# Performance work log

Measured on AMD Instinct MI355X. Metric: run time of the kernel, lower is better.

Reference implementation:

```python
import jax, jax.numpy as jnp
import numpy as np
from jax import lax

B, L, DIN, DOUT, K = 8, 4096, 256, 256, 3


def _gates(x, W, b, k):
    # x: [B, L, Din] -> conv over time, channels-first like torch Conv1d
    xt = jnp.transpose(x, (0, 2, 1))  # [B, Din, L]
    pad = (k - 1) // 2
    g = lax.conv_general_dilated(xt, W, window_strides=(1,), padding=[(pad, pad)],
                                 dimension_numbers=("NCH", "OIH", "NCH"))
    g = g + b[None, :, None]
    g = jnp.transpose(g, (0, 2, 1))  # [B, L, 3*Dout]
    f, o, z = jnp.split(g, 3, axis=-1)
    return jax.nn.sigmoid(f), jax.nn.sigmoid(o), jnp.tanh(z)


def _fo_pool(f, z, init_cell, reverse):
    # c_t = f_t * c_{t-1} + (1 - f_t) * z_t ; scan over time axis
    fT = jnp.transpose(f, (1, 0, 2))  # [L, B, D]
    zT = jnp.transpose(z, (1, 0, 2))

    def step(c, fz):
        ft, zt = fz
        c = ft * c + (1.0 - ft) * zt
        return c, c

    _, cells = lax.scan(step, init_cell, (fT, zT), reverse=reverse)
    return jnp.transpose(cells, (1, 0, 2))  # [B, L, D]


def setup_inputs() -> dict:
    key = jax.random.key(0)
    k1, k2, k3, k4, k5, k6 = jax.random.split(key, 6)
    scale_in = 1.0 / np.sqrt(DIN * K)
    inp = {
        "input": jax.random.normal(k1, (B, L, DIN), dtype=jnp.float32),
        "lengths": jnp.full((B,), L, dtype=jnp.int64) if False else jax.random.randint(k2, (B,), 1, L + 1),
        "W_fwd": jax.random.uniform(k3, (3 * DOUT, DIN, K), dtype=jnp.float32, minval=-scale_in, maxval=scale_in),
        "b_fwd": jax.random.uniform(k4, (3 * DOUT,), dtype=jnp.float32, minval=-scale_in, maxval=scale_in),
        "W_bwd": jax.random.uniform(k5, (3 * DOUT, DIN, K), dtype=jnp.float32, minval=-scale_in, maxval=scale_in),
        "b_bwd": jax.random.uniform(k6, (3 * DOUT,), dtype=jnp.float32, minval=-scale_in, maxval=scale_in),
    }
    return inp


def reference(input, lengths, W_fwd, b_fwd, W_bwd, b_bwd):
    init_cell = jnp.zeros((input.shape[0], DOUT), dtype=input.dtype)

    # forward direction
    f, o, z = _gates(input, W_fwd, b_fwd, K)
    cell = _fo_pool(f, z, init_cell, reverse=False)
    hidden = cell * o

    # backward direction
    fr, orr, zr = _gates(input, W_bwd, b_bwd, K)
    rcell = _fo_pool(fr, zr, init_cell, reverse=True)
    rhidden = rcell * orr

    output = jnp.concatenate([hidden, rhidden], axis=-1)  # [B, L, 2*Dout]
    last_h = jnp.concatenate([hidden[:, -1, :], rhidden[:, -1, :]], axis=-1)
    last_c = jnp.concatenate([cell[:, -1, :], rcell[:, -1, :]], axis=-1)
    return output, last_h, last_c
```

## Files before the change

kernel.cpp:

```cpp
#include <hip/hip_runtime.h>
#include <hip/hip_bf16.h>
#include <hip/hip_fp16.h>

#define B_     8
#define L_     4096
#define DIN    256
#define DOUT   256
#define NGATE  1536
#define KDIM   768
#define LP     (L_ + 2)
#define CHUNK  32
#define NCHUNK (L_ / CHUNK)

typedef short    short8  __attribute__((ext_vector_type(8)));
typedef __bf16   bf16x8  __attribute__((ext_vector_type(8)));
typedef float    floatx4 __attribute__((ext_vector_type(4)));
typedef _Float16 half4   __attribute__((ext_vector_type(4)));

__device__ __forceinline__ float fast_sigmoid(float x) {
    return __builtin_amdgcn_rcpf(1.f + __expf(-x));
}
__device__ __forceinline__ float fast_tanh(float x) {
    return 1.f - 2.f * __builtin_amdgcn_rcpf(1.f + __expf(2.f * x));
}
__device__ __forceinline__ unsigned short f2bf(float x) {
    unsigned u = __float_as_uint(x);
    u += 0x7FFF + ((u >> 16) & 1);
    return (unsigned short)(u >> 16);
}
__device__ __forceinline__ void gload16(const unsigned short* g, unsigned short* l) {
    __builtin_amdgcn_global_load_lds((const __attribute__((address_space(1))) void*)g,
                                     (__attribute__((address_space(3))) void*)l,
                                     16, 0, 0);
}

__device__ __forceinline__ int gate_noff(int n) {
    return (n >> 7) * 32768 + ((n >> 6) & 1) * 4096 + ((n >> 4) & 3) * 1024 + (n & 15) * 4;
}
__device__ __forceinline__ int gate_toff(int b, int t) {
    return (b * 16 + (t >> 8)) * 393216 + ((t >> 6) & 3) * 8192
         + ((t >> 4) & 3) * 256 + ((t >> 2) & 3) * 64;
}

#define NXB ((B_ * LP * 64 + 255) / 256)
#define NWB ((NGATE * KDIM + 255) / 256)
__global__ void prep_all(const float* __restrict__ x, unsigned short* __restrict__ Xp,
                         const float* __restrict__ Wf, const float* __restrict__ bf_,
                         const float* __restrict__ Wb, const float* __restrict__ bb,
                         unsigned short* __restrict__ Wc, float* __restrict__ bc) {
    if (blockIdx.x < NXB) {
        int idx = blockIdx.x * 256 + threadIdx.x;
        int row = idx >> 6;
        if (row >= B_ * LP) return;
        int c4 = (idx & 63) << 2;
        int b = row / LP, r = row - b * LP;
        float4 v = make_float4(0.f, 0.f, 0.f, 0.f);
        if (r >= 1 && r <= L_) {
            v = *(const float4*)(x + ((size_t)(b * L_ + (r - 1))) * DIN + c4);
        }
        ushort4 o = make_ushort4(f2bf(v.x), f2bf(v.y), f2bf(v.z), f2bf(v.w));
        *(ushort4*)(Xp + (size_t)row * DIN + c4) = o;
    } else {
        int gid = (blockIdx.x - NXB) * 256 + threadIdx.x;
        if (gid < NGATE) {
            bc[gid] = (gid < 768) ? bf_[gid] : bb[gid - 768];
        }
        if (gid >= NGATE * KDIM) return;
        int n = gid / KDIM, k = gid - n * KDIM;
        int s = k >> 8, ic = k & 255;
        const float* W = (n < 768) ? Wf : Wb;
        int oc = (n < 768) ? n : n - 768;
        float v = W[(size_t)oc * KDIM + ic * 3 + s];
        Wc[(size_t)n * KDIM + k] = f2bf(v);
    }
}

__launch_bounds__(512)
__global__ void gemm_gates(const unsigned short* __restrict__ Xp,
                           const unsigned short* __restrict__ Wc,
                           const float* __restrict__ bc,
                           _Float16* __restrict__ gates) {
    __shared__ unsigned short As[256 * 64];
    __shared__ unsigned short Bs[128 * 64];
    const int tid  = threadIdx.x;
    const int lane = tid & 63, wave = tid >> 6;
    const int quad = lane >> 4, l16 = lane & 15;
    const int wr = wave >> 1, wcl = wave & 1;

    int flat = blockIdx.x;
    int xcd  = flat & 7;
    int slot = flat >> 3;
    int bm   = xcd * 16 + slot / 12;
    int nblk = slot % 12;
    const int b  = bm >> 4;
    const int t0 = (bm & 15) << 8;
    const int n0 = nblk << 7;
    const unsigned short* Ab = Xp + (size_t)b * LP * DIN;

    int rowA[4], cgA[4], rowB[2], cgB[2];
#pragma unroll
    for (int j = 0; j < 4; j++) {
        int G = (wave * 4 + j) * 64 + lane;
        rowA[j] = G >> 3;
        cgA[j]  = ((G & 7) ^ (rowA[j] & 7)) * 8;
    }
#pragma unroll
    for (int j = 0; j < 2; j++) {
        int G = (wave * 2 + j) * 64 + lane;
        rowB[j] = G >> 3;
        cgB[j]  = ((G & 7) ^ (rowB[j] & 7)) * 8;
    }

    floatx4 acc[4][4];
#pragma unroll
    for (int i = 0; i < 4; i++)
#pragma unroll
        for (int j = 0; j < 4; j++) acc[i][j] = (floatx4)0.f;

    for (int k0 = 0; k0 < KDIM; k0 += 64) {
        const int sh = k0 >> 8;
        const int c0 = k0 & 255;
#pragma unroll
        for (int j = 0; j < 4; j++)
            gload16(Ab + (size_t)(t0 + rowA[j] + sh) * DIN + c0 + cgA[j],
                    &As[(wave * 4 + j) * 512]);
#pragma unroll
        for (int j = 0; j < 2; j++)
            gload16(Wc + (size_t)(n0 + rowB[j]) * KDIM + k0 + cgB[j],
                    &Bs[(wave * 2 + j) * 512]);
        __syncthreads();
#pragma unroll
        for (int kk = 0; kk < 2; kk++) {
            const int g0 = kk * 4 + quad;
            short8 af[4], bfr[4];
#pragma unroll
            for (int mi = 0; mi < 4; mi++) {
                int row = wr * 64 + mi * 16 + l16;
                af[mi] = *(const short8*)&As[row * 64 + ((g0 ^ (row & 7)) << 3)];
            }
#pragma unroll
            for (int ni = 0; ni < 4; ni++) {
                int row = wcl * 64 + ni * 16 + l16;
                bfr[ni] = *(const short8*)&Bs[row * 64 + ((g0 ^ (row & 7)) << 3)];
            }
#pragma unroll
            for (int mi = 0; mi < 4; mi++)
#pragma unroll
                for (int ni = 0; ni < 4; ni++)
                    acc[mi][ni] = __builtin_amdgcn_mfma_f32_16x16x32_bf16(
                        __builtin_bit_cast(bf16x8, af[mi]),
                        __builtin_bit_cast(bf16x8, bfr[ni]),
                        acc[mi][ni], 0, 0, 0);
        }
        __syncthreads();
    }

    const int cls = ((n0 + wcl * 64) >> 8) % 3;
    _Float16* gb = gates + ((size_t)(bm * 12 + nblk) * 8 + wave) * 4096 + lane * 4;
#pragma unroll
    for (int ni = 0; ni < 4; ni++) {
        float bias = bc[n0 + wcl * 64 + ni * 16 + l16];
#pragma unroll
        for (int mi = 0; mi < 4; mi++) {
            half4 hv;
#pragma unroll
            for (int rr = 0; rr < 4; rr++) {
                float v = acc[mi][ni][rr] + bias;
                v = (cls == 2) ? fast_tanh(v) : fast_sigmoid(v);
                hv[rr] = (_Float16)v;
            }
            *(half4*)(gb + (ni * 4 + mi) * 256) = hv;
        }
    }
}

__global__ void scan_chunks(const _Float16* __restrict__ gates,
                            float2* __restrict__ PW) {
    const int d = threadIdx.x;
    const int s = blockIdx.x, b = blockIdx.y, dir = blockIdx.z;
    const int onf = gate_noff(dir * 768 + d);
    const int onz = gate_noff(dir * 768 + 512 + d);
    float P = 1.f, W = 0.f;
    if (dir == 0) {
#pragma unroll
        for (int gi = 0; gi < 8; gi++) {
            int t = s * CHUNK + gi * 4;
            int ot = gate_toff(b, t);
            half4 f4 = *(const half4*)(gates + ot + onf);
            half4 z4 = *(const half4*)(gates + ot + onz);
#pragma unroll
            for (int u = 0; u < 4; u++) {
                float f = (float)f4[u], z = (float)z4[u];
                W = f * W + (1.f - f) * z;
                P *= f;
            }
        }
    } else {
#pragma unroll
        for (int gi = 7; gi >= 0; gi--) {
            int t = s * CHUNK + gi * 4;
            int ot = gate_toff(b, t);
            half4 f4 = *(const half4*)(gates + ot + onf);
            half4 z4 = *(const half4*)(gates + ot + onz);
#pragma unroll
            for (int u = 3; u >= 0; u--) {
                float f = (float)f4[u], z = (float)z4[u];
                W = f * W + (1.f - f) * z;
                P *= f;
            }
        }
    }
    PW[(((size_t)(dir * 8 + b)) * NCHUNK + s) * 256 + d] = make_float2(P, W);
}

__global__ void scan_seq(const float2* __restrict__ PW, float* __restrict__ C0) {
    const int c = threadIdx.x;
    const int dir = blockIdx.x >> 3, b = blockIdx.x & 7;
    const size_t base = ((size_t)(dir * 8 + b)) * NCHUNK * 256 + c;
    float cc = 0.f;
    if (dir == 0) {
#pragma unroll 16
        for (int s = 0; s < NCHUNK; s++) {
            float2 pw = PW[base + (size_t)s * 256];
            C0[base + (size_t)s * 256] = cc;
            cc = pw.x * cc + pw.y;
        }
    } else {
#pragma unroll 16
        for (int s = NCHUNK - 1; s >= 0; s--) {
            float2 pw = PW[base + (size_t)s * 256];
            C0[base + (size_t)s * 256] = cc;
            cc = pw.x * cc + pw.y;
        }
    }
}

__global__ void scan_final(const _Float16* __restrict__ gates,
                           const float* __restrict__ C0,
                           float* __restrict__ out) {
    __shared__ float hbuf[CHUNK][256];
    const int d = threadIdx.x;
    const int s = blockIdx.x, b = blockIdx.y, dir = blockIdx.z;
    const int onf = gate_noff(dir * 768 + d);
    const int ono = gate_noff(dir * 768 + 256 + d);
    const int onz = gate_noff(dir * 768 + 512 + d);
    float c = C0[(((size_t)(dir * 8 + b)) * NCHUNK + s) * 256 + d];
    float* ob = out + (size_t)(b * L_) * (2 * DOUT) + dir * DOUT;
    float* lasth = out + (size_t)B_ * L_ * (2 * DOUT);
    float* lastc = lasth + B_ * (2 * DOUT);

#pragma unroll
    for (int gg = 0; gg < 8; gg++) {
        int gi = (dir == 0) ? gg : 7 - gg;
        int t = s * CHUNK + gi * 4;
        int ot = gate_toff(b, t);
        half4 f4 = *(const half4*)(gates + ot + onf);
        half4 o4 = *(const half4*)(gates + ot + ono);
        half4 z4 = *(const half4*)(gates + ot + onz);
        if (dir == 0) {
#pragma unroll
            for (int u = 0; u < 4; u++) {
                float f = (float)f4[u], z = (float)z4[u];
                c = f * c + (1.f - f) * z;
                float h = c * (float)o4[u];
                hbuf[gi * 4 + u][d] = h;
                if (s == NCHUNK - 1 && gi == 7 && u == 3) {
                    lasth[b * 2 * DOUT + d] = h;
                    lastc[b * 2 * DOUT + d] = c;
                }
            }
        } else {
#pragma unroll
            for (int u = 3; u >= 0; u--) {
                float f = (float)f4[u], z = (float)z4[u];
                c = f * c + (1.f - f) * z;
                float h = c * (float)o4[u];
                hbuf[gi * 4 + u][d] = h;
                if (u == 3 && s == NCHUNK - 1 && gi == 7) {
                    lasth[b * 2 * DOUT + DOUT + d] = h;
                    lastc[b * 2 * DOUT + DOUT + d] = c;
                }
            }
        }
    }
    __syncthreads();
#pragma unroll
    for (int u = 0; u < 8; u++) {
        int slot = u * 256 + d;
        int row = slot >> 6, col = (slot & 63) << 2;
        *(float4*)&ob[(size_t)(s * CHUNK + row) * (2 * DOUT) + col] =
            *(float4*)&hbuf[row][col];
    }
}

extern "C" void kernel_launch(void* const* d_in, const int* in_sizes, int n_in,
                              void* d_out, int out_size, void* d_ws, size_t ws_size,
                              hipStream_t stream) {
    const float* x   = (const float*)d_in[0];
    const float* Wf  = (const float*)d_in[2];
    const float* bfv = (const float*)d_in[3];
    const float* Wb  = (const float*)d_in[4];
    const float* bbv = (const float*)d_in[5];

    char* ws = (char*)d_ws;
    unsigned short* Xp    = (unsigned short*)(ws);
    unsigned short* Wc    = (unsigned short*)(ws + 16785408);
    float*          bc    = (float*)(ws + 19144704);
    _Float16*       gates = (_Float16*)(ws + 19150848);
    float2*         PW    = (float2*)(ws);
    float*          C0    = (float*)(ws + 4194304);
    float*          out   = (float*)d_out;

    prep_all<<<NXB + NWB, 256, 0, stream>>>(x, Xp, Wf, bfv, Wb, bbv, Wc, bc);
    gemm_gates<<<1536, 512, 0, stream>>>(Xp, Wc, bc, gates);
    scan_chunks<<<dim3(NCHUNK, B_, 2), 256, 0, stream>>>(gates, PW);
    scan_seq<<<16, 256, 0, stream>>>(PW, C0);
    scan_final<<<dim3(NCHUNK, B_, 2), 256, 0, stream>>>(gates, C0, out);
}
```

Measured before the change: 221.6 us.

## Fuse chunk-level scan summaries into gate GEMM epilogue with interleaved f/z columns

After: 212.0 us. 1.05x faster.

```diff
diff --git a/kernel.cpp b/kernel.cpp
--- a/kernel.cpp
+++ b/kernel.cpp
@@ -34,12 +34,35 @@
                                      16, 0, 0);
 }
 
-__device__ __forceinline__ int gate_noff(int n) {
-    return (n >> 7) * 32768 + ((n >> 6) & 1) * 4096 + ((n >> 4) & 3) * 1024 + (n & 15) * 4;
-}
-__device__ __forceinline__ int gate_toff(int b, int t) {
+__device__ __forceinline__ int toff_g(int b, int t) {
     return (b * 16 + (t >> 8)) * 393216 + ((t >> 6) & 3) * 8192
          + ((t >> 4) & 3) * 256 + ((t >> 2) & 3) * 64;
+}
+__device__ __forceinline__ int noff_f(int dir, int d) {
+    int nblk = dir * 6 + (d >> 6);
+    int wcl = (d >> 5) & 1, jb = (d >> 4) & 1, l16 = d & 15;
+    return nblk * 32768 + wcl * 4096 + (jb * 2) * 1024 + l16 * 4;
+}
+__device__ __forceinline__ int noff_z(int dir, int d) {
+    int nblk = dir * 6 + (d >> 6);
+    int wcl = (d >> 5) & 1, jb = (d >> 4) & 1, l16 = d & 15;
+    return nblk * 32768 + wcl * 4096 + (jb * 2 + 1) * 1024 + l16 * 4;
+}
+__device__ __forceinline__ int noff_o(int dir, int d) {
+    int nblk = dir * 6 + 4 + (d >> 7);
+    int c7 = d & 127;
+    int wcl = c7 >> 6, ni = (c7 >> 4) & 3, l16 = d & 15;
+    return nblk * 32768 + wcl * 4096 + ni * 1024 + l16 * 4;
+}
+__device__ __forceinline__ int col_to_oc(int n, int* dir_out) {
+    int nb = n >> 7, c = n & 127;
+    int dir = nb / 6, r = nb % 6;
+    int wcl = (c >> 6) & 1, ni = (c >> 4) & 3, l16 = c & 15;
+    int oc;
+    if (r < 4) oc = ((ni & 1) ? 512 : 0) + r * 64 + wcl * 32 + (ni >> 1) * 16 + l16;
+    else       oc = 256 + (r - 4) * 128 + c;
+    *dir_out = dir;
+    return oc;
 }
 
 #define NXB ((B_ * LP * 64 + 255) / 256)
@@ -63,13 +86,16 @@
     } else {
         int gid = (blockIdx.x - NXB) * 256 + threadIdx.x;
         if (gid < NGATE) {
-            bc[gid] = (gid < 768) ? bf_[gid] : bb[gid - 768];
+            int dirb;
+            int oc = col_to_oc(gid, &dirb);
+            bc[gid] = dirb ? bb[oc] : bf_[oc];
         }
         if (gid >= NGATE * KDIM) return;
         int n = gid / KDIM, k = gid - n * KDIM;
         int s = k >> 8, ic = k & 255;
-        const float* W = (n < 768) ? Wf : Wb;
-        int oc = (n < 768) ? n : n - 768;
+        int dirb;
+        int oc = col_to_oc(n, &dirb);
+        const float* W = dirb ? Wb : Wf;
         float v = W[(size_t)oc * KDIM + ic * 3 + s];
         Wc[(size_t)n * KDIM + k] = f2bf(v);
     }
@@ -79,7 +105,8 @@
 __global__ void gemm_gates(const unsigned short* __restrict__ Xp,
                            const unsigned short* __restrict__ Wc,
                            const float* __restrict__ bc,
-                           _Float16* __restrict__ gates) {
+                           _Float16* __restrict__ gates,
+                           float2* __restrict__ PWp) {
     __shared__ unsigned short As[256 * 64];
     __shared__ unsigned short Bs[128 * 64];
     const int tid  = threadIdx.x;
@@ -155,62 +182,78 @@
         __syncthreads();
     }
 
-    const int cls = ((n0 + wcl * 64) >> 8) % 3;
+    const int dir = nblk / 6;
+    const int r6  = nblk % 6;
     _Float16* gb = gates + ((size_t)(bm * 12 + nblk) * 8 + wave) * 4096 + lane * 4;
-#pragma unroll
-    for (int ni = 0; ni < 4; ni++) {
-        float bias = bc[n0 + wcl * 64 + ni * 16 + l16];
-#pragma unroll
-        for (int mi = 0; mi < 4; mi++) {
-            half4 hv;
-#pragma unroll
-            for (int rr = 0; rr < 4; rr++) {
-                float v = acc[mi][ni][rr] + bias;
-                v = (cls == 2) ? fast_tanh(v) : fast_sigmoid(v);
-                hv[rr] = (_Float16)v;
-            }
-            *(half4*)(gb + (ni * 4 + mi) * 256) = hv;
-        }
-    }
-}
-
-__global__ void scan_chunks(const _Float16* __restrict__ gates,
-                            float2* __restrict__ PW) {
-    const int d = threadIdx.x;
-    const int s = blockIdx.x, b = blockIdx.y, dir = blockIdx.z;
-    const int onf = gate_noff(dir * 768 + d);
-    const int onz = gate_noff(dir * 768 + 512 + d);
-    float P = 1.f, W = 0.f;
-    if (dir == 0) {
-#pragma unroll
-        for (int gi = 0; gi < 8; gi++) {
-            int t = s * CHUNK + gi * 4;
-            int ot = gate_toff(b, t);
-            half4 f4 = *(const half4*)(gates + ot + onf);
-            half4 z4 = *(const half4*)(gates + ot + onz);
-#pragma unroll
-            for (int u = 0; u < 4; u++) {
-                float f = (float)f4[u], z = (float)z4[u];
-                W = f * W + (1.f - f) * z;
-                P *= f;
+
+    if (r6 >= 4) {
+#pragma unroll
+        for (int ni = 0; ni < 4; ni++) {
+            float bias = bc[n0 + wcl * 64 + ni * 16 + l16];
+#pragma unroll
+            for (int mi = 0; mi < 4; mi++) {
+                half4 hv;
+#pragma unroll
+                for (int rr = 0; rr < 4; rr++)
+                    hv[rr] = (_Float16)fast_sigmoid(acc[mi][ni][rr] + bias);
+                *(half4*)(gb + (ni * 4 + mi) * 256) = hv;
             }
         }
     } else {
-#pragma unroll
-        for (int gi = 7; gi >= 0; gi--) {
-            int t = s * CHUNK + gi * 4;
-            int ot = gate_toff(b, t);
-            half4 f4 = *(const half4*)(gates + ot + onf);
-            half4 z4 = *(const half4*)(gates + ot + onz);
-#pragma unroll
-            for (int u = 3; u >= 0; u--) {
-                float f = (float)f4[u], z = (float)z4[u];
-                W = f * W + (1.f - f) * z;
-                P *= f;
-            }
-        }
-    }
-    PW[(((size_t)(dir * 8 + b)) * NCHUNK + s) * 256 + d] = make_float2(P, W);
+        const bool fwd = (dir == 0);
+#pragma unroll
+        for (int j = 0; j < 2; j++) {
+            float biasF = bc[n0 + wcl * 64 + (2 * j) * 16 + l16];
+            float biasZ = bc[n0 + wcl * 64 + (2 * j + 1) * 16 + l16];
+            float Pm[4], Wm[4];
+#pragma unroll
+            for (int mi = 0; mi < 4; mi++) {
+                half4 hf, hz;
+                float P = 1.f, W = 0.f;
+                if (fwd) {
+#pragma unroll
+                    for (int rr = 0; rr < 4; rr++) {
+                        float f = fast_sigmoid(acc[mi][2 * j][rr] + biasF);
+                        float z = fast_tanh(acc[mi][2 * j + 1][rr] + biasZ);
+                        hf[rr] = (_Float16)f; hz[rr] = (_Float16)z;
+                        W = f * W + (1.f - f) * z; P *= f;
+                    }
+                } else {
+#pragma unroll
+                    for (int rr = 3; rr >= 0; rr--) {
+                        float f = fast_sigmoid(acc[mi][2 * j][rr] + biasF);
+                        float z = fast_tanh(acc[mi][2 * j + 1][rr] + biasZ);
+                        hf[rr] = (_Float16)f; hz[rr] = (_Float16)z;
+                        W = f * W + (1.f - f) * z; P *= f;
+                    }
+                }
+                *(half4*)(gb + ((2 * j) * 4 + mi) * 256) = hf;
+                *(half4*)(gb + ((2 * j + 1) * 4 + mi) * 256) = hz;
+#pragma unroll
+                for (int st = 0; st < 2; st++) {
+                    int msk = 16 << st;
+                    float Po = __shfl_xor(P, msk);
+                    float Wo = __shfl_xor(W, msk);
+                    bool later = (((lane & msk) != 0) == fwd);
+                    float nP = later ? (P * Po) : (Po * P);
+                    float nW = later ? (P * Wo + W) : (Po * W + Wo);
+                    P = nP; W = nW;
+                }
+                Pm[mi] = P; Wm[mi] = W;
+            }
+            if (quad < 2) {
+                int half = quad;
+                int mlo = half * 2, mhi = half * 2 + 1;
+                float Pc, Wc2;
+                if (fwd) { Pc = Pm[mhi] * Pm[mlo]; Wc2 = Pm[mhi] * Wm[mlo] + Wm[mhi]; }
+                else     { Pc = Pm[mlo] * Pm[mhi]; Wc2 = Pm[mlo] * Wm[mhi] + Wm[mlo]; }
+                int s  = (bm & 15) * 8 + wr * 2 + half;
+                int ch = r6 * 64 + wcl * 32 + j * 16 + l16;
+                PWp[(((size_t)(dir * 8 + b)) * NCHUNK + s) * 256 + ch] =
+                    make_float2(Pc, Wc2);
+            }
+        }
+    }
 }
 
 __global__ void scan_seq(const float2* __restrict__ PW, float* __restrict__ C0) {
@@ -241,9 +284,9 @@
     __shared__ float hbuf[CHUNK][256];
     const int d = threadIdx.x;
     const int s = blockIdx.x, b = blockIdx.y, dir = blockIdx.z;
-    const int onf = gate_noff(dir * 768 + d);
-    const int ono = gate_noff(dir * 768 + 256 + d);
-    const int onz = gate_noff(dir * 768 + 512 + d);
+    const int onf = noff_f(dir, d);
+    const int ono = noff_o(dir, d);
+    const int onz = noff_z(dir, d);
     float c = C0[(((size_t)(dir * 8 + b)) * NCHUNK + s) * 256 + d];
     float* ob = out + (size_t)(b * L_) * (2 * DOUT) + dir * DOUT;
     float* lasth = out + (size_t)B_ * L_ * (2 * DOUT);
@@ -253,7 +296,7 @@
     for (int gg = 0; gg < 8; gg++) {
         int gi = (dir == 0) ? gg : 7 - gg;
         int t = s * CHUNK + gi * 4;
-        int ot = gate_toff(b, t);
+        int ot = toff_g(b, t);
         half4 f4 = *(const half4*)(gates + ot + onf);
         half4 o4 = *(const half4*)(gates + ot + ono);
         half4 z4 = *(const half4*)(gates + ot + onz);
@@ -307,13 +350,12 @@
     unsigned short* Wc    = (unsigned short*)(ws + 16785408);
     float*          bc    = (float*)(ws + 19144704);
     _Float16*       gates = (_Float16*)(ws + 19150848);
-    float2*         PW    = (float2*)(ws);
     float*          C0    = (float*)(ws + 4194304);
+    float2*         PW    = (float2*)d_out;
     float*          out   = (float*)d_out;
 
     prep_all<<<NXB + NWB, 256, 0, stream>>>(x, Xp, Wf, bfv, Wb, bbv, Wc, bc);
-    gemm_gates<<<1536, 512, 0, stream>>>(Xp, Wc, bc, gates);
-    scan_chunks<<<dim3(NCHUNK, B_, 2), 256, 0, stream>>>(gates, PW);
+    gemm_gates<<<1536, 512, 0, stream>>>(Xp, Wc, bc, gates, PW);
     scan_seq<<<16, 256, 0, stream>>>(PW, C0);
     scan_final<<<dim3(NCHUNK, B_, 2), 256, 0, stream>>>(gates, C0, out);
 }
```
